# Kernel tuning notes

Measured on AMD Instinct MI355X. Metric: run time of the kernel, lower is better.

Reference implementation:

```python
import jax, jax.numpy as jnp
import numpy as np

ANGLE = 0.5  # angular margin from init_kwargs


def setup_inputs() -> dict:
    key = jax.random.key(0)
    k1, k2, k3 = jax.random.split(key, 3)
    B, F, C = 512, 128, 100000
    # scale by 0.1 so exp(features @ w) and exp(modulus * cos) stay finite in fp32
    features = jax.random.normal(k1, (B, F), dtype=jnp.float32) * 0.1
    w = jax.random.normal(k2, (F, C), dtype=jnp.float32) * 0.1
    target = jax.random.randint(k3, (B,), 0, C, dtype=jnp.int64)
    return {"features": features, "w": w, "target": target}


def reference(features, w, target):
    B = features.shape[0]
    rows = jnp.arange(B)
    # norms: [B,1] and [1,C]
    features_modulus = jnp.sqrt(jnp.sum(features ** 2, axis=1, keepdims=True))
    w_modulus = jnp.sqrt(jnp.sum(w ** 2, axis=0, keepdims=True))
    modulus = features_modulus * w_modulus  # [B, C]
    logits = jnp.matmul(features, w)  # [B, C] (computed once; torch computes it twice)
    cos_theta = logits / modulus / 1.01
    theta = jnp.arccos(cos_theta) + ANGLE
    cos_theta_plus = jnp.cos(theta)
    margin_logits = modulus * cos_theta_plus  # [B, C]
    top = jnp.exp(margin_logits[rows, target])  # [B]
    down_ = jnp.exp(logits)  # [B, C]
    down = jnp.sum(down_, axis=1) - down_[rows, target] + top  # [B]
    return -jnp.sum(jnp.log(top / down)) / B
```

## Files before the change

### kernel.cpp

```cpp
#include <hip/hip_runtime.h>

#define F_DIM 128
#define C_DIM 100000
#define B_ROWS 512
#define ANGLE 0.5f
#define NXB 196
#define COLS_PER_BLK 512

typedef __attribute__((ext_vector_type(4))) float  f32x4;
typedef __attribute__((ext_vector_type(8))) short  bf16x8;
typedef __attribute__((ext_vector_type(4))) short  bf16x4;

static __device__ __forceinline__ unsigned short f2bf(float x) {
    unsigned int u = __float_as_uint(x);
    u += 0x7FFFu + ((u >> 16) & 1u);
    return (unsigned short)(u >> 16);
}

__global__ __launch_bounds__(256, 2)
void arc_main(const float* __restrict__ feat,
              const float* __restrict__ w,
              float* __restrict__ pp)
{
    __shared__ unsigned short lA[128 * 128];
    __shared__ unsigned short lB[128 * 128];
    __shared__ float lRow[128];

    const int tid    = threadIdx.x;
    const int r0     = blockIdx.x * 128;
    const int cblk   = blockIdx.y;
    const int cbase0 = cblk * COLS_PER_BLK;

    if (tid < 128) lRow[tid] = 0.f;

    #pragma unroll
    for (int it = 0; it < 16; ++it) {
        const int idx4 = it * 256 + tid;
        const int row  = idx4 >> 5;
        const int c4   = idx4 & 31;
        const f32x4 v  = *(const f32x4*)(feat + (size_t)(r0 + row) * F_DIM + c4 * 4);
        bf16x4 h;
        h[0] = (short)f2bf(v[0]); h[1] = (short)f2bf(v[1]);
        h[2] = (short)f2bf(v[2]); h[3] = (short)f2bf(v[3]);
        const int pc   = (c4 >> 1) ^ (row & 15);
        const int half = c4 & 1;
        *(bf16x4*)&lA[row * 128 + pc * 8 + half * 4] = h;
    }

    const int lane = tid & 63;
    const int wv   = tid >> 6;
    const int quad = lane >> 4;
    const int l15  = lane & 15;
    const int nb   = wv * 32;

    float esum[8][4];
    #pragma unroll
    for (int m = 0; m < 8; ++m)
        #pragma unroll
        for (int r = 0; r < 4; ++r) esum[m][r] = 0.f;

    for (int t = 0; t < 4; ++t) {
        const int cbase = cbase0 + t * 128;

        #pragma unroll
        for (int it = 0; it < 16; ++it) {
            const int idx4 = it * 256 + tid;
            const int k    = idx4 >> 5;
            const int c4   = idx4 & 31;
            const int c    = cbase + c4 * 4;
            f32x4 v = {0.f, 0.f, 0.f, 0.f};
            if (c < C_DIM)
                v = *(const f32x4*)(w + (size_t)k * C_DIM + c);
            bf16x4 h;
            h[0] = (short)f2bf(v[0]); h[1] = (short)f2bf(v[1]);
            h[2] = (short)f2bf(v[2]); h[3] = (short)f2bf(v[3]);
            *(bf16x4*)&lB[k * 128 + c4 * 4] = h;
        }
        __syncthreads();

        f32x4 acc[8][2];
        #pragma unroll
        for (int m = 0; m < 8; ++m) {
            acc[m][0] = (f32x4){0.f, 0.f, 0.f, 0.f};
            acc[m][1] = (f32x4){0.f, 0.f, 0.f, 0.f};
        }

        #pragma unroll
        for (int ks = 0; ks < 4; ++ks) {
            bf16x8 bfr[2];
            #pragma unroll
            for (int s = 0; s < 2; ++s) {
                #pragma unroll
                for (int j = 0; j < 8; ++j)
                    bfr[s][j] = (short)lB[(ks * 32 + quad * 8 + j) * 128 + nb + s * 16 + l15];
            }
            #pragma unroll
            for (int m = 0; m < 8; ++m) {
                const int row = m * 16 + l15;
                const int pc  = (ks * 4 + quad) ^ (row & 15);
                const bf16x8 af = *(const bf16x8*)&lA[row * 128 + pc * 8];
                acc[m][0] = __builtin_amdgcn_mfma_f32_16x16x32_bf16(af, bfr[0], acc[m][0], 0, 0, 0);
                acc[m][1] = __builtin_amdgcn_mfma_f32_16x16x32_bf16(af, bfr[1], acc[m][1], 0, 0, 0);
            }
        }

        const int  col0 = cbase + nb + l15;
        const int  col1 = col0 + 16;
        const bool v0   = col0 < C_DIM;
        const bool v1   = col1 < C_DIM;
        #pragma unroll
        for (int m = 0; m < 8; ++m) {
            #pragma unroll
            for (int r = 0; r < 4; ++r) {
                if (v0) esum[m][r] += __expf(acc[m][0][r]);
                if (v1) esum[m][r] += __expf(acc[m][1][r]);
            }
        }
        __syncthreads();
    }

    #pragma unroll
    for (int m = 0; m < 8; ++m) {
        #pragma unroll
        for (int r = 0; r < 4; ++r) {
            float s = esum[m][r];
            #pragma unroll
            for (int off = 1; off < 16; off <<= 1)
                s += __shfl_xor(s, off);
            if (l15 == 0)
                atomicAdd(&lRow[m * 16 + quad * 4 + r], s);
        }
    }
    __syncthreads();
    if (tid < 128)
        pp[(size_t)(r0 + tid) * NXB + cblk] = lRow[tid];
}

__global__ void arc_row(const float* __restrict__ feat,
                        const float* __restrict__ w,
                        const int*   __restrict__ target,
                        const float* __restrict__ pp,
                        float* __restrict__ term)
{
    const int b    = blockIdx.x;
    const int lane = threadIdx.x;
    const int t    = target[b];

    float dot = 0.f, wsq = 0.f, fsq = 0.f, rs = 0.f;
    #pragma unroll
    for (int h = 0; h < 2; ++h) {
        const int f  = lane + h * 64;
        const float fv = feat[b * F_DIM + f];
        const float wv = w[(size_t)f * C_DIM + t];
        dot += fv * wv;
        wsq += wv * wv;
        fsq += fv * fv;
    }
    for (int j = lane; j < NXB; j += 64)
        rs += pp[(size_t)b * NXB + j];

    #pragma unroll
    for (int off = 32; off > 0; off >>= 1) {
        dot += __shfl_xor(dot, off);
        wsq += __shfl_xor(wsq, off);
        fsq += __shfl_xor(fsq, off);
        rs  += __shfl_xor(rs,  off);
    }
    if (lane == 0) {
        const float mod = sqrtf(fsq) * sqrtf(wsq);
        float ct = dot / (mod * 1.01f);
        ct = fminf(1.f, fmaxf(-1.f, ct));
        const float th   = acosf(ct) + ANGLE;
        const float marg = mod * cosf(th);
        const float down = rs - expf(dot) + expf(marg);
        term[b] = marg - logf(down);
    }
}

__global__ void arc_loss(const float* __restrict__ term,
                         float* __restrict__ out)
{
    __shared__ float red[B_ROWS];
    const int b = threadIdx.x;
    red[b] = term[b];
    __syncthreads();
    #pragma unroll
    for (int st = 256; st > 0; st >>= 1) {
        if (b < st) red[b] += red[b + st];
        __syncthreads();
    }
    if (b == 0) out[0] = -red[0] / (float)B_ROWS;
}

extern "C" void kernel_launch(void* const* d_in, const int* in_sizes, int n_in,
                              void* d_out, int out_size, void* d_ws, size_t ws_size,
                              hipStream_t stream)
{
    const float* feat   = (const float*)d_in[0];
    const float* w      = (const float*)d_in[1];
    const int*   target = (const int*)d_in[2];

    float* pp   = (float*)d_ws;
    float* term = pp + (size_t)B_ROWS * NXB;

    arc_main<<<dim3(4, NXB), 256, 0, stream>>>(feat, w, pp);
    arc_row<<<B_ROWS, 64, 0, stream>>>(feat, w, target, pp, term);
    arc_loss<<<1, B_ROWS, 0, stream>>>(term, (float*)d_out);
}
```

Measured before the change: 144.0 us.

## Restructure main kernel so each block covers all rows for one column tile

The main kernel now launches one 1024-thread block per 128-column tile of w. Each block covers all 512 feature rows: the features sit in registers as MFMA B fragments and the transposed, padded w tile sits in LDS. Each w element is now read from global memory once instead of once per 128-row chunk, and the explicit row tiling, atomics and per-block reduction buffer go away. Out-of-range columns are left as zeros, so each adds exp(0)=1 to the row sum; the row kernel subtracts a constant 96 to correct for this. The trade-offs are that every block re-reads all features from global memory, and the row kernel's partial-sum reads become strided.

```diff
diff --git a/kernel.cpp b/kernel.cpp
--- a/kernel.cpp
+++ b/kernel.cpp
@@ -4,136 +4,96 @@
 #define C_DIM 100000
 #define B_ROWS 512
 #define ANGLE 0.5f
-#define NXB 196
-#define COLS_PER_BLK 512
+#define CPB 128
+#define NCB 782
+#define OOB_PAD 96.0f
+#define LBT_S 136
 
 typedef __attribute__((ext_vector_type(4))) float  f32x4;
 typedef __attribute__((ext_vector_type(8))) short  bf16x8;
 typedef __attribute__((ext_vector_type(4))) short  bf16x4;
 
-static __device__ __forceinline__ unsigned short f2bf(float x) {
+static __device__ __forceinline__ short f2bf(float x) {
     unsigned int u = __float_as_uint(x);
     u += 0x7FFFu + ((u >> 16) & 1u);
-    return (unsigned short)(u >> 16);
+    return (short)(u >> 16);
 }
 
-__global__ __launch_bounds__(256, 2)
+__global__ __launch_bounds__(1024, 4)
 void arc_main(const float* __restrict__ feat,
               const float* __restrict__ w,
               float* __restrict__ pp)
 {
-    __shared__ unsigned short lA[128 * 128];
-    __shared__ unsigned short lB[128 * 128];
-    __shared__ float lRow[128];
+    __shared__ unsigned short lBt[128 * LBT_S];
 
-    const int tid    = threadIdx.x;
-    const int r0     = blockIdx.x * 128;
-    const int cblk   = blockIdx.y;
-    const int cbase0 = cblk * COLS_PER_BLK;
+    const int tid = threadIdx.x;
+    const int cb  = blockIdx.x;
+    const int c0  = cb * CPB;
 
-    if (tid < 128) lRow[tid] = 0.f;
-
-    #pragma unroll
-    for (int it = 0; it < 16; ++it) {
-        const int idx4 = it * 256 + tid;
-        const int row  = idx4 >> 5;
-        const int c4   = idx4 & 31;
-        const f32x4 v  = *(const f32x4*)(feat + (size_t)(r0 + row) * F_DIM + c4 * 4);
-        bf16x4 h;
-        h[0] = (short)f2bf(v[0]); h[1] = (short)f2bf(v[1]);
-        h[2] = (short)f2bf(v[2]); h[3] = (short)f2bf(v[3]);
-        const int pc   = (c4 >> 1) ^ (row & 15);
-        const int half = c4 & 1;
-        *(bf16x4*)&lA[row * 128 + pc * 8 + half * 4] = h;
+    {
+        const int c  = tid & 127;
+        const int g  = tid >> 7;
+        const int gc = c0 + c;
+        float v[16];
+        #pragma unroll
+        for (int i = 0; i < 16; ++i)
+            v[i] = (gc < C_DIM) ? w[(size_t)(g * 16 + i) * C_DIM + gc] : 0.f;
+        #pragma unroll
+        for (int j = 0; j < 4; ++j) {
+            bf16x4 h;
+            h[0] = f2bf(v[4*j+0]); h[1] = f2bf(v[4*j+1]);
+            h[2] = f2bf(v[4*j+2]); h[3] = f2bf(v[4*j+3]);
+            *(bf16x4*)&lBt[c * LBT_S + g * 16 + j * 4] = h;
+        }
     }
 
     const int lane = tid & 63;
     const int wv   = tid >> 6;
     const int quad = lane >> 4;
     const int l15  = lane & 15;
-    const int nb   = wv * 32;
 
-    float esum[8][4];
+    bf16x8 fB[2][4];
     #pragma unroll
-    for (int m = 0; m < 8; ++m)
-        #pragma unroll
-        for (int r = 0; r < 4; ++r) esum[m][r] = 0.f;
-
-    for (int t = 0; t < 4; ++t) {
-        const int cbase = cbase0 + t * 128;
-
-        #pragma unroll
-        for (int it = 0; it < 16; ++it) {
-            const int idx4 = it * 256 + tid;
-            const int k    = idx4 >> 5;
-            const int c4   = idx4 & 31;
-            const int c    = cbase + c4 * 4;
-            f32x4 v = {0.f, 0.f, 0.f, 0.f};
-            if (c < C_DIM)
-                v = *(const f32x4*)(w + (size_t)k * C_DIM + c);
-            bf16x4 h;
-            h[0] = (short)f2bf(v[0]); h[1] = (short)f2bf(v[1]);
-            h[2] = (short)f2bf(v[2]); h[3] = (short)f2bf(v[3]);
-            *(bf16x4*)&lB[k * 128 + c4 * 4] = h;
-        }
-        __syncthreads();
-
-        f32x4 acc[8][2];
-        #pragma unroll
-        for (int m = 0; m < 8; ++m) {
-            acc[m][0] = (f32x4){0.f, 0.f, 0.f, 0.f};
-            acc[m][1] = (f32x4){0.f, 0.f, 0.f, 0.f};
-        }
-
+    for (int s = 0; s < 2; ++s) {
+        const int b = wv * 32 + s * 16 + l15;
         #pragma unroll
         for (int ks = 0; ks < 4; ++ks) {
-            bf16x8 bfr[2];
-            #pragma unroll
-            for (int s = 0; s < 2; ++s) {
-                #pragma unroll
-                for (int j = 0; j < 8; ++j)
-                    bfr[s][j] = (short)lB[(ks * 32 + quad * 8 + j) * 128 + nb + s * 16 + l15];
-            }
-            #pragma unroll
-            for (int m = 0; m < 8; ++m) {
-                const int row = m * 16 + l15;
-                const int pc  = (ks * 4 + quad) ^ (row & 15);
-                const bf16x8 af = *(const bf16x8*)&lA[row * 128 + pc * 8];
-                acc[m][0] = __builtin_amdgcn_mfma_f32_16x16x32_bf16(af, bfr[0], acc[m][0], 0, 0, 0);
-                acc[m][1] = __builtin_amdgcn_mfma_f32_16x16x32_bf16(af, bfr[1], acc[m][1], 0, 0, 0);
-            }
-        }
-
-        const int  col0 = cbase + nb + l15;
-        const int  col1 = col0 + 16;
-        const bool v0   = col0 < C_DIM;
-        const bool v1   = col1 < C_DIM;
-        #pragma unroll
-        for (int m = 0; m < 8; ++m) {
-            #pragma unroll
-            for (int r = 0; r < 4; ++r) {
-                if (v0) esum[m][r] += __expf(acc[m][0][r]);
-                if (v1) esum[m][r] += __expf(acc[m][1][r]);
-            }
-        }
-        __syncthreads();
-    }
-
-    #pragma unroll
-    for (int m = 0; m < 8; ++m) {
-        #pragma unroll
-        for (int r = 0; r < 4; ++r) {
-            float s = esum[m][r];
-            #pragma unroll
-            for (int off = 1; off < 16; off <<= 1)
-                s += __shfl_xor(s, off);
-            if (l15 == 0)
-                atomicAdd(&lRow[m * 16 + quad * 4 + r], s);
+            const int k0 = ks * 32 + quad * 8;
+            const f32x4 u0 = *(const f32x4*)(feat + b * F_DIM + k0);
+            const f32x4 u1 = *(const f32x4*)(feat + b * F_DIM + k0 + 4);
+            bf16x8 h;
+            h[0] = f2bf(u0[0]); h[1] = f2bf(u0[1]); h[2] = f2bf(u0[2]); h[3] = f2bf(u0[3]);
+            h[4] = f2bf(u1[0]); h[5] = f2bf(u1[1]); h[6] = f2bf(u1[2]); h[7] = f2bf(u1[3]);
+            fB[s][ks] = h;
         }
     }
     __syncthreads();
-    if (tid < 128)
-        pp[(size_t)(r0 + tid) * NXB + cblk] = lRow[tid];
+
+    float esum0 = 0.f, esum1 = 0.f;
+    #pragma unroll
+    for (int m = 0; m < 8; ++m) {
+        f32x4 a0 = {0.f, 0.f, 0.f, 0.f};
+        f32x4 a1 = {0.f, 0.f, 0.f, 0.f};
+        #pragma unroll
+        for (int ks = 0; ks < 4; ++ks) {
+            const bf16x8 af =
+                *(const bf16x8*)&lBt[(m * 16 + l15) * LBT_S + ks * 32 + quad * 8];
+            a0 = __builtin_amdgcn_mfma_f32_16x16x32_bf16(af, fB[0][ks], a0, 0, 0, 0);
+            a1 = __builtin_amdgcn_mfma_f32_16x16x32_bf16(af, fB[1][ks], a1, 0, 0, 0);
+        }
+        #pragma unroll
+        for (int r = 0; r < 4; ++r) {
+            esum0 += __expf(a0[r]);
+            esum1 += __expf(a1[r]);
+        }
+    }
+
+    esum0 += __shfl_xor(esum0, 16); esum0 += __shfl_xor(esum0, 32);
+    esum1 += __shfl_xor(esum1, 16); esum1 += __shfl_xor(esum1, 32);
+    if (lane < 16) {
+        pp[(size_t)cb * 512 + wv * 32 + lane]      = esum0;
+        pp[(size_t)cb * 512 + wv * 32 + 16 + lane] = esum1;
+    }
 }
 
 __global__ void arc_row(const float* __restrict__ feat,
@@ -156,8 +116,8 @@
         wsq += wv * wv;
         fsq += fv * fv;
     }
-    for (int j = lane; j < NXB; j += 64)
-        rs += pp[(size_t)b * NXB + j];
+    for (int j = lane; j < NCB; j += 64)
+        rs += pp[(size_t)j * 512 + b];
 
     #pragma unroll
     for (int off = 32; off > 0; off >>= 1) {
@@ -172,7 +132,7 @@
         ct = fminf(1.f, fmaxf(-1.f, ct));
         const float th   = acosf(ct) + ANGLE;
         const float marg = mod * cosf(th);
-        const float down = rs - expf(dot) + expf(marg);
+        const float down = rs - OOB_PAD - expf(dot) + expf(marg);
         term[b] = marg - logf(down);
     }
 }
@@ -201,9 +161,9 @@
     const int*   target = (const int*)d_in[2];
 
     float* pp   = (float*)d_ws;
-    float* term = pp + (size_t)B_ROWS * NXB;
+    float* term = pp + (size_t)NCB * 512;
 
-    arc_main<<<dim3(4, NXB), 256, 0, stream>>>(feat, w, pp);
+    arc_main<<<NCB, 1024, 0, stream>>>(feat, w, pp);
     arc_row<<<B_ROWS, 64, 0, stream>>>(feat, w, target, pp, term);
     arc_loss<<<1, B_ROWS, 0, stream>>>(term, (float*)d_out);
 }
```

Measured after the change: 135.8 us. 1.06x faster.
